# Optimization experiments

Hardware: AMD Instinct MI355X
Metric: run time of the kernel (lower is better)

Reference implementation:

```python
import jax, jax.numpy as jnp
import numpy as np

B, S, D, H, WIN = 2, 2048, 1024, 16, 512
DK = D // H
NEG_INF = float('-inf')


def setup_inputs() -> dict:
    key = jax.random.key(0)
    ks = jax.random.split(key, 9)
    sc = 1.0 / np.sqrt(D)
    def w(k):
        return jax.random.normal(k, (D, D), jnp.float32) * sc
    def b(k):
        return jax.random.normal(k, (D,), jnp.float32) * 0.01
    return {
        'x': jax.random.normal(ks[0], (B, S, D), jnp.float32),
        'Wq_w': w(ks[1]), 'Wq_b': b(jax.random.fold_in(ks[1], 1)),
        'Wk_w': w(ks[2]), 'Wk_b': b(jax.random.fold_in(ks[2], 1)),
        'Wv_w': w(ks[3]), 'Wv_b': b(jax.random.fold_in(ks[3], 1)),
        'Wo_w': w(ks[4]), 'Wo_b': b(jax.random.fold_in(ks[4], 1)),
    }


def _sliding_window_softmax(scores):
    """Faithful port of _apply_sliding_window_attention.

    scores: [B, H, S, S]. seq_len is a multiple of WIN (padding_len == 0,
    which is the only case where the original torch code runs without a
    shape error). Reshape rows/cols into WIN-sized blocks, apply the full
    causal mask (viewed block-wise), softmax over the within-window key
    axis, reshape back. Rows whose entire window block is masked produce
    NaN in torch; here they are defined as 0 (safe softmax) so the
    reference is numerically usable.
    """
    b, h, s, _ = scores.shape
    nb = s // WIN
    causal = jnp.tril(jnp.ones((s, s), dtype=bool)).reshape(1, 1, nb, WIN, nb, WIN)
    sc = scores.reshape(b, h, nb, WIN, nb, WIN)
    sc = jnp.where(causal, sc, NEG_INF)
    m = jnp.max(sc, axis=-1, keepdims=True)
    e = jnp.exp(sc - jnp.where(jnp.isfinite(m), m, 0.0))
    e = jnp.where(causal, e, 0.0)
    denom = jnp.sum(e, axis=-1, keepdims=True)
    probs = e / jnp.where(denom == 0.0, 1.0, denom)
    return probs.reshape(b, h, s, s)


def reference(x, Wq_w, Wq_b, Wk_w, Wk_b, Wv_w, Wv_b, Wo_w, Wo_b):
    b, s, d = x.shape
    # torch nn.Linear: y = x @ W.T + b
    q = (x @ Wq_w.T + Wq_b).reshape(b, s, H, DK).transpose(0, 2, 1, 3)  # [B,H,S,DK]
    k = (x @ Wk_w.T + Wk_b).reshape(b, s, H, DK).transpose(0, 2, 1, 3)
    v = (x @ Wv_w.T + Wv_b).reshape(b, s, H, DK).transpose(0, 2, 1, 3)

    attn_scores = jnp.einsum('bhqd,bhkd->bhqk', q, k) / np.sqrt(DK)  # [B,H,S,S]
    if WIN < s:  # sliding-window branch (window softmax, as in the source)
        attn_scores = _sliding_window_softmax(attn_scores)
    # second, full-row softmax (the source applies softmax again)
    attn_probs = jax.nn.softmax(attn_scores, axis=-1)
    attn_out = jnp.einsum('bhqk,bhkd->bhqd', attn_probs, v)
    attn_out = attn_out.transpose(0, 2, 1, 3).reshape(b, s, d)
    return attn_out @ Wo_w.T + Wo_b
```

## Files before the change

kernel.cpp:

```cpp
#include <hip/hip_runtime.h>
#include <hip/hip_bf16.h>

typedef short v8s __attribute__((ext_vector_type(8)));
typedef float v4f __attribute__((ext_vector_type(4)));
typedef unsigned int v4u __attribute__((ext_vector_type(4)));
typedef unsigned int v2u __attribute__((ext_vector_type(2)));

#define DEV static __device__ __forceinline__
#define AS1 __attribute__((address_space(1)))
#define AS3 __attribute__((address_space(3)))

DEV float bf2f(unsigned short u){ unsigned int x=((unsigned int)u)<<16; float f; __builtin_memcpy(&f,&x,4); return f; }
DEV short f2bf(float f){ __hip_bfloat16 h=__float2bfloat16(f); short s; __builtin_memcpy(&s,&h,2); return s; }
DEV unsigned int f2bfu(float f){ unsigned int u; __builtin_memcpy(&u,&f,4); return (u + 0x7fffu + ((u>>16)&1u)) >> 16; }
DEV unsigned int pk2(float a, float b){ return f2bfu(a) | (f2bfu(b)<<16); }
DEV v4f mfma16(v8s a, v8s b, v4f c){ return __builtin_amdgcn_mfma_f32_16x16x32_bf16(a,b,c,0,0,0); }
DEV float fexp2(float x){
#if __has_builtin(__builtin_amdgcn_exp2f)
  return __builtin_amdgcn_exp2f(x);
#else
  float r; asm("v_exp_f32 %0, %1" : "=v"(r) : "v"(x)); return r;
#endif
}

__global__ __launch_bounds__(256) void convert_kernel(
    const float* __restrict__ x,  const float* __restrict__ Wq,
    const float* __restrict__ Wk, const float* __restrict__ Wv,
    short* __restrict__ xb, short* __restrict__ wqb,
    short* __restrict__ wkb, short* __restrict__ wvb)
{
  unsigned g = blockIdx.x*256u + threadIdx.x;
  const float* src; short* dst; unsigned off;
  if (g < 1048576u){ src=x;  dst=xb;  off=g; }
  else if (g < 1310720u){ src=Wq; dst=wqb; off=g-1048576u; }
  else if (g < 1572864u){ src=Wk; dst=wkb; off=g-1310720u; }
  else { src=Wv; dst=wvb; off=g-1572864u; }
  v4f f = *(const v4f*)(src + (size_t)off*4);
  v2u r; r[0]=pk2(f[0],f[1]); r[1]=pk2(f[2],f[3]);
  *(v2u*)(dst + (size_t)off*4) = r;
}

__global__ __launch_bounds__(256) void convertW_kernel(const float* __restrict__ src,
                                                       short* __restrict__ dst)
{
  unsigned off = blockIdx.x*256u + threadIdx.x;
  v4f f = *(const v4f*)(src + (size_t)off*4);
  v2u r; r[0]=pk2(f[0],f[1]); r[1]=pk2(f[2],f[3]);
  *(v2u*)(dst + (size_t)off*4) = r;
}

DEV void gemm_core16(const short* __restrict__ A, const short* __restrict__ Bmat,
                     int brow0, int bn0, int tid, short* As, short* Bs, v4f acc[4][4])
{
  const int l = tid & 63, w = tid >> 6;
  const int wr = (w>>1)*64, wc = (w&1)*64;
  const int row = tid>>2, p = tid&3;
  const int sw = (p^((row>>1)&3))*8;
  auto STAGE=[&](int kt,int buf){
    const short* a0 = A    + (size_t)(brow0+row   )*1024 + kt*32 + sw;
    const short* a1 = A    + (size_t)(brow0+row+64)*1024 + kt*32 + sw;
    const short* b0 = Bmat + (size_t)(bn0 +row   )*1024 + kt*32 + sw;
    const short* b1 = Bmat + (size_t)(bn0 +row+64)*1024 + kt*32 + sw;
    __builtin_amdgcn_global_load_lds((const AS1 void*)a0,(AS3 void*)(As+buf*4096+(size_t)tid*8),16,0,0);
    __builtin_amdgcn_global_load_lds((const AS1 void*)a1,(AS3 void*)(As+buf*4096+(size_t)(tid+256)*8),16,0,0);
    __builtin_amdgcn_global_load_lds((const AS1 void*)b0,(AS3 void*)(Bs+buf*4096+(size_t)tid*8),16,0,0);
    __builtin_amdgcn_global_load_lds((const AS1 void*)b1,(AS3 void*)(Bs+buf*4096+(size_t)(tid+256)*8),16,0,0);
  };
  STAGE(0,0);
  asm volatile("s_waitcnt vmcnt(0)" ::: "memory");
  __builtin_amdgcn_s_barrier();
  int cur=0;
  for (int kt=0; kt<32; ++kt){
    if (kt<31) STAGE(kt+1,cur^1);
    v8s af[4], bfr[4];
    #pragma unroll
    for (int m=0;m<4;++m){ int r=wr+m*16+(l&15); af[m]=*(const v8s*)&As[cur*4096+(r*4+((l>>4)^((r>>1)&3)))*8]; }
    #pragma unroll
    for (int n=0;n<4;++n){ int r=wc+n*16+(l&15); bfr[n]=*(const v8s*)&Bs[cur*4096+(r*4+((l>>4)^((r>>1)&3)))*8]; }
    #pragma unroll
    for (int m=0;m<4;++m)
      #pragma unroll
      for (int n=0;n<4;++n)
        acc[m][n]=mfma16(af[m],bfr[n],acc[m][n]);
    asm volatile("s_waitcnt vmcnt(0)" ::: "memory");
    __builtin_amdgcn_s_barrier();
    cur^=1;
  }
}

__global__ __launch_bounds__(256) void qkv_gemm(const short* __restrict__ xb,
    const short* __restrict__ wqb, const short* __restrict__ wkb, const short* __restrict__ wvb,
    const float* __restrict__ bq, const float* __restrict__ bk, const float* __restrict__ bv,
    short* __restrict__ qo, short* __restrict__ ko, short* __restrict__ vfo)
{
  __shared__ short As[8192], Bs[8192];
  const int tid=threadIdx.x, l=tid&63, w=tid>>6;
  const int bcol0=blockIdx.x*128, brow0=blockIdx.y*128;
  const int mat=bcol0>>10, n0=bcol0&1023;
  const short* Wm   = mat==0?wqb:(mat==1?wkb:wvb);
  const float* bias = mat==0?bq:(mat==1?bk:bv);
  v4f acc[4][4];
  v4f vz={0.f,0.f,0.f,0.f};
  #pragma unroll
  for(int m=0;m<4;++m)
    #pragma unroll
    for(int n=0;n<4;++n) acc[m][n]=vz;
  gemm_core16(xb, Wm, brow0, n0, tid, As, Bs, acc);
  const int wr=(w>>1)*64, wc=(w&1)*64;
  const float qscale = 0.18033688011112042f;
  #pragma unroll
  for(int m=0;m<4;++m)
  #pragma unroll
  for(int n=0;n<4;++n)
  #pragma unroll
  for(int r=0;r<4;++r){
    int row=brow0+wr+m*16+(l>>4)*4+r;
    int col=n0+wc+n*16+(l&15);
    float v=acc[m][n][r]+bias[col];
    int b=row>>11, s=row&2047, h=col>>6, dk=col&63;
    int bh=b*16+h;
    if(mat==0)      qo[((size_t)bh*2048+s)*64+dk]=f2bf(v*qscale);
    else if(mat==1) ko[((size_t)bh*2048+s)*64+dk]=f2bf(v);
    else{
      int kb=s>>9, c=(s>>5)&15, ki=s&31;
      int g2=(ki>>2)&3, j=(ki>>4)*4+(ki&3);
      int lane2=g2*16+(dk&15);
      vfo[((((size_t)bh*4+kb)*16+c)*4+(size_t)(dk>>4))*512 + lane2*8 + j]=f2bf(v);
    }
  }
}

__global__ __launch_bounds__(256) void vbsum_kernel(const short* __restrict__ vf, float* __restrict__ vbp)
{
  __shared__ float red[4][4][16];
  const int bh=blockIdx.x, kb=blockIdx.y, tid=threadIdx.x, wv=tid>>6, l=tid&63;
  const short* base = vf + ((size_t)(bh*4+kb))*16*4*512;
  float acc[4]={0.f,0.f,0.f,0.f};
  #pragma unroll
  for(int cc=0;cc<4;++cc){
    int c=wv*4+cc;
    #pragma unroll
    for(int dt=0;dt<4;++dt){
      v8s vv=*(const v8s*)(base + ((size_t)(c*4+dt))*512 + l*8);
      float s=0.f;
      #pragma unroll
      for(int j=0;j<8;++j) s+=bf2f((unsigned short)vv[j]);
      acc[dt]+=s;
    }
  }
  #pragma unroll
  for(int dt=0;dt<4;++dt){
    acc[dt]+=__shfl_xor(acc[dt],16);
    acc[dt]+=__shfl_xor(acc[dt],32);
  }
  if(l<16){
    #pragma unroll
    for(int dt=0;dt<4;++dt) red[wv][dt][l]=acc[dt];
  }
  __syncthreads();
  if(tid<64){
    int dt=tid>>4, d=tid&15;
    float s=(red[0][dt][d]+red[1][dt][d])+(red[2][dt][d]+red[3][dt][d]);
    vbp[(size_t)(bh*4+kb)*64 + dt*16 + d]=s;
  }
}

__global__ __launch_bounds__(256) void attn_kernel(
  const short* __restrict__ q, const short* __restrict__ k, const short* __restrict__ vf,
  const float* __restrict__ vbp, short* __restrict__ attn)
{
  __shared__ short kbuf[16384];
  __shared__ float d1buf[256];
  const int tid=threadIdx.x, l=tid&63, wv=tid>>6;
  const int bh=blockIdx.x, qt=31-blockIdx.y;
  const int qb=qt>>3;
  const int qrow0=qt*64+wv*16;
  const int g=l>>4, q16=l&15;
  const int b=bh>>4, h=bh&15;
  const int qglob=qrow0+q16;
  const int lrow=wv*16+q16;

  const short* qbase = q + (size_t)bh*2048*64;
  const short* kbase = k + (size_t)bh*2048*64;
  const short* qp = qbase + (size_t)(qrow0+q16)*64 + g*8;
  v8s qa0=*(const v8s*)qp, qa1=*(const v8s*)(qp+32);
  v4f vz={0.f,0.f,0.f,0.f};

  auto stage=[&](int kb2,int hb2){
    #pragma unroll
    for (int i=0;i<8;++i){
      int idx=i*256+tid, key=idx>>3, p=idx&7, pp=p^(key&7);
      const short* gp = kbase + (size_t)(kb2*512+hb2*256+key)*64 + pp*8;
      __builtin_amdgcn_global_load_lds((const AS1 void*)gp,
          (AS3 void*)((char*)kbuf + idx*16), 16, 0, 0);
    }
  };

#define QKE(CT, EV)                                                     \
  v4f EV;                                                               \
  { int krow=((CT)&15)*16+q16;                                          \
    int s0=g^(krow&7), s1=(g+4)^(krow&7);                               \
    v8s k0=*(const v8s*)&kbuf[(krow*8+s0)*8];                           \
    v8s k1=*(const v8s*)&kbuf[(krow*8+s1)*8];                           \
    __builtin_amdgcn_s_setprio(1);                                      \
    v4f t=mfma16(k0,qa0,vz);                                            \
    v4f e4=mfma16(k1,qa1,t);                                            \
    __builtin_amdgcn_s_setprio(0);                                      \
    _Pragma("unroll")                                                   \
    for (int r=0;r<4;++r){                                              \
      float s=e4[r];                                                    \
      if (diag && kb*512+(CT)*16+g*4+r > qglob) s=-1e38f;               \
      EV[r]=fexp2(s);                                                   \
    }                                                                   \
  }

  for (int kb=0; kb<=qb; ++kb){
    const bool diag=(kb==qb);
    const int tmaxw = diag ? ((qt&7)*4+wv) : 31;
    const int blkhi = diag ? ((qt&7)*4+3) : 31;
    float d1acc=0.f;
    stage(kb,0); __syncthreads();
    #pragma unroll
    for (int ct=0;ct<16;++ct) if (ct<=tmaxw){
      QKE(ct,ev)
      d1acc+=(ev[0]+ev[1])+(ev[2]+ev[3]);
    }
    __syncthreads();
    if (blkhi>=16){
      stage(kb,1); __syncthreads();
      #pragma unroll
      for (int ct=16;ct<32;++ct) if (ct<=tmaxw){
        QKE(ct,ev)
        d1acc+=(ev[0]+ev[1])+(ev[2]+ev[3]);
      }
      __syncthreads();
    }
    float d1=d1acc;
    d1+=__shfl_xor(d1,16); d1+=__shfl_xor(d1,32);
    if (l<16) d1buf[(wv*16+l)*4+kb]=1.44269504f/d1;
  }
  __syncthreads();

  v4f o[4];
  #pragma unroll
  for(int dt=0;dt<4;++dt) o[dt]=vz;
  float zacc=0.f;

#define CHUNK(C)                                                        \
  { QKE(2*(C),eA) QKE(2*(C)+1,eB)                                       \
    float w0=fexp2(eA[0]*d1i)-1.0f, w1=fexp2(eA[1]*d1i)-1.0f;           \
    float w2=fexp2(eA[2]*d1i)-1.0f, w3=fexp2(eA[3]*d1i)-1.0f;           \
    float w4=fexp2(eB[0]*d1i)-1.0f, w5=fexp2(eB[1]*d1i)-1.0f;           \
    float w6=fexp2(eB[2]*d1i)-1.0f, w7=fexp2(eB[3]*d1i)-1.0f;           \
    zacc+=((w0+w1)+(w2+w3))+((w4+w5)+(w6+w7));                          \
    union { v4u u; v8s s; } pa;                                         \
    pa.u[0]=pk2(w0,w1); pa.u[1]=pk2(w2,w3);                             \
    pa.u[2]=pk2(w4,w5); pa.u[3]=pk2(w6,w7);                             \
    const short* vfp = vf + ((((size_t)bh*4+kb)*16+(C))*4)*512 + l*8;   \
    __builtin_amdgcn_s_setprio(1);                                      \
    _Pragma("unroll")                                                   \
    for (int dt=0;dt<4;++dt){                                           \
      v8s vfr=*(const v8s*)(vfp + (size_t)dt*512);                      \
      o[dt]=mfma16(pa.s,vfr,o[dt]);                                     \
    }                                                                   \
    __builtin_amdgcn_s_setprio(0);                                      \
  }

  for (int kb=0; kb<=qb; ++kb){
    const bool diag=(kb==qb);
    const int tmaxw = diag ? ((qt&7)*4+wv) : 31;
    const int blkhi = diag ? ((qt&7)*4+3) : 31;
    const float d1i=d1buf[lrow*4+kb];
    stage(kb,0); __syncthreads();
    #pragma unroll
    for (int c=0;c<8;++c) if (2*c<=tmaxw) CHUNK(c)
    __syncthreads();
    if (blkhi>=16){
      stage(kb,1); __syncthreads();
      #pragma unroll
      for (int c=8;c<16;++c) if (2*c<=tmaxw) CHUNK(c)
      __syncthreads();
    }
  }
#undef CHUNK
#undef QKE

  float z=zacc;
  z+=__shfl_xor(z,16); z+=__shfl_xor(z,32);
  float base[4];
  #pragma unroll
  for (int dt=0;dt<4;++dt){
    float s=0.f;
    #pragma unroll
    for (int kk=0;kk<4;++kk) s+=vbp[(size_t)(bh*4+kk)*64 + dt*16 + q16];
    base[dt]=s;
  }
  #pragma unroll
  for (int r=0;r<4;++r){
    float zr=__shfl(z, g*4+r);
    float inv=1.0f/(2048.0f+zr);
    int rowi=qrow0+g*4+r;
    size_t obase=((size_t)b*2048+rowi)*1024 + h*64;
    #pragma unroll
    for (int dt=0;dt<4;++dt)
      attn[obase + dt*16 + q16] = f2bf((o[dt][r]+base[dt])*inv);
  }
}

__global__ __launch_bounds__(256) void oproj_gemm(const short* __restrict__ at,
    const short* __restrict__ wob, const float* __restrict__ bo, float* __restrict__ out)
{
  __shared__ short As[8192], Bs[8192];
  const int tid=threadIdx.x, l=tid&63, w=tid>>6;
  const int bcol0=blockIdx.x*128, brow0=blockIdx.y*128;
  v4f acc[4][4];
  v4f vz={0.f,0.f,0.f,0.f};
  #pragma unroll
  for(int m=0;m<4;++m)
    #pragma unroll
    for(int n=0;n<4;++n) acc[m][n]=vz;
  gemm_core16(at, wob, brow0, bcol0, tid, As, Bs, acc);
  const int wr=(w>>1)*64, wc=(w&1)*64;
  #pragma unroll
  for(int m=0;m<4;++m)
  #pragma unroll
  for(int n=0;n<4;++n)
  #pragma unroll
  for(int r=0;r<4;++r){
    int row=brow0+wr+m*16+(l>>4)*4+r;
    int col=bcol0+wc+n*16+(l&15);
    out[(size_t)row*1024+col]=acc[m][n][r]+bo[col];
  }
}

extern "C" void kernel_launch(void* const* d_in, const int* in_sizes, int n_in,
                              void* d_out, int out_size, void* d_ws, size_t ws_size,
                              hipStream_t stream)
{
  const float* x  =(const float*)d_in[0];
  const float* Wq =(const float*)d_in[1];
  const float* bq =(const float*)d_in[2];
  const float* Wk =(const float*)d_in[3];
  const float* bk =(const float*)d_in[4];
  const float* Wv =(const float*)d_in[5];
  const float* bv =(const float*)d_in[6];
  const float* Wo =(const float*)d_in[7];
  const float* bo =(const float*)d_in[8];
  float* out=(float*)d_out;
  char* ws=(char*)d_ws;
  short* xb_ws =(short*)(ws);
  short* at_ws =(short*)(ws);
  short* q_ws  =(short*)(ws + ((size_t)8<<20));
  short* wob_ws=(short*)(ws + ((size_t)8<<20));
  short* k_ws  =(short*)(ws + ((size_t)16<<20));
  short* vf_ws =(short*)(ws + ((size_t)24<<20));
  char*  outb  =(char*)d_out;
  short* wqb   =(short*)(outb);
  short* wkb   =(short*)(outb + ((size_t)2<<20));
  short* wvb   =(short*)(outb + ((size_t)4<<20));
  float* vbp_ws=(float*)(outb + ((size_t)7<<20));

  convert_kernel<<<dim3(7168),256,0,stream>>>(x,Wq,Wk,Wv,xb_ws,wqb,wkb,wvb);
  qkv_gemm<<<dim3(24,32),256,0,stream>>>(xb_ws,wqb,wkb,wvb,bq,bk,bv,q_ws,k_ws,vf_ws);
  vbsum_kernel<<<dim3(32,4),256,0,stream>>>(vf_ws,vbp_ws);
  attn_kernel<<<dim3(32,32),256,0,stream>>>(q_ws,k_ws,vf_ws,vbp_ws,at_ws);
  convertW_kernel<<<dim3(1024),256,0,stream>>>(Wo,wob_ws);
  oproj_gemm<<<dim3(8,32),256,0,stream>>>(at_ws,wob_ws,bo,out);
}
```

Baseline: 152.1 us.

## Cache window scores in registers as bf16 instead of recomputing QK in second pass

The attention kernel previously ran two passes over each key window: one computing QK^T and exp to get the row denominators, and a second recomputing QK^T to build the PV weights. Now the single pass keeps the exponentiated scores packed as bf16 in a 64-entry register array, reduces the denominator, then runs PV directly from the cached values. This removes half the K staging, barriers and QK MFMAs, and also drops the s_setprio hints. In exchange it adds heavy register pressure (64 extra VGPRs, possibly spilling to scratch or lowering occupancy) and rounds the intermediate scores to bf16 before the second exponent.

```diff
diff --git a/kernel.cpp b/kernel.cpp
--- a/kernel.cpp
+++ b/kernel.cpp
@@ -170,7 +170,6 @@
   const float* __restrict__ vbp, short* __restrict__ attn)
 {
   __shared__ short kbuf[16384];
-  __shared__ float d1buf[256];
   const int tid=threadIdx.x, l=tid&63, wv=tid>>6;
   const int bh=blockIdx.x, qt=31-blockIdx.y;
   const int qb=qt>>3;
@@ -178,7 +177,6 @@
   const int g=l>>4, q16=l&15;
   const int b=bh>>4, h=bh&15;
   const int qglob=qrow0+q16;
-  const int lrow=wv*16+q16;
 
   const short* qbase = q + (size_t)bh*2048*64;
   const short* kbase = k + (size_t)bh*2048*64;
@@ -196,94 +194,76 @@
     }
   };
 
-#define QKE(CT, EV)                                                     \
-  v4f EV;                                                               \
+  v4f o[4];
+  #pragma unroll
+  for(int dt=0;dt<4;++dt) o[dt]=vz;
+  float zacc=0.f;
+  unsigned sc16[64];
+
+#define QKE(CT)                                                         \
   { int krow=((CT)&15)*16+q16;                                          \
     int s0=g^(krow&7), s1=(g+4)^(krow&7);                               \
     v8s k0=*(const v8s*)&kbuf[(krow*8+s0)*8];                           \
     v8s k1=*(const v8s*)&kbuf[(krow*8+s1)*8];                           \
-    __builtin_amdgcn_s_setprio(1);                                      \
     v4f t=mfma16(k0,qa0,vz);                                            \
     v4f e4=mfma16(k1,qa1,t);                                            \
-    __builtin_amdgcn_s_setprio(0);                                      \
+    v4f ev;                                                             \
     _Pragma("unroll")                                                   \
     for (int r=0;r<4;++r){                                              \
       float s=e4[r];                                                    \
       if (diag && kb*512+(CT)*16+g*4+r > qglob) s=-1e38f;               \
-      EV[r]=fexp2(s);                                                   \
+      ev[r]=fexp2(s);                                                   \
+      d1acc+=ev[r];                                                     \
     }                                                                   \
-  }
-
-  for (int kb=0; kb<=qb; ++kb){
-    const bool diag=(kb==qb);
-    const int tmaxw = diag ? ((qt&7)*4+wv) : 31;
-    const int blkhi = diag ? ((qt&7)*4+3) : 31;
-    float d1acc=0.f;
-    stage(kb,0); __syncthreads();
-    #pragma unroll
-    for (int ct=0;ct<16;++ct) if (ct<=tmaxw){
-      QKE(ct,ev)
-      d1acc+=(ev[0]+ev[1])+(ev[2]+ev[3]);
-    }
-    __syncthreads();
-    if (blkhi>=16){
-      stage(kb,1); __syncthreads();
-      #pragma unroll
-      for (int ct=16;ct<32;++ct) if (ct<=tmaxw){
-        QKE(ct,ev)
-        d1acc+=(ev[0]+ev[1])+(ev[2]+ev[3]);
-      }
-      __syncthreads();
-    }
-    float d1=d1acc;
-    d1+=__shfl_xor(d1,16); d1+=__shfl_xor(d1,32);
-    if (l<16) d1buf[(wv*16+l)*4+kb]=1.44269504f/d1;
-  }
-  __syncthreads();
-
-  v4f o[4];
-  #pragma unroll
-  for(int dt=0;dt<4;++dt) o[dt]=vz;
-  float zacc=0.f;
-
-#define CHUNK(C)                                                        \
-  { QKE(2*(C),eA) QKE(2*(C)+1,eB)                                       \
-    float w0=fexp2(eA[0]*d1i)-1.0f, w1=fexp2(eA[1]*d1i)-1.0f;           \
-    float w2=fexp2(eA[2]*d1i)-1.0f, w3=fexp2(eA[3]*d1i)-1.0f;           \
-    float w4=fexp2(eB[0]*d1i)-1.0f, w5=fexp2(eB[1]*d1i)-1.0f;           \
-    float w6=fexp2(eB[2]*d1i)-1.0f, w7=fexp2(eB[3]*d1i)-1.0f;           \
+    sc16[(CT)*2]=pk2(ev[0],ev[1]); sc16[(CT)*2+1]=pk2(ev[2],ev[3]);     \
+  }
+
+#define PVC(C)                                                          \
+  { unsigned a0=sc16[4*(C)], a1=sc16[4*(C)+1];                          \
+    unsigned b0=sc16[4*(C)+2], b1=sc16[4*(C)+3];                        \
+    float w0=fexp2(bf2f((unsigned short)(a0&0xffffu))*d1i)-1.0f;        \
+    float w1=fexp2(bf2f((unsigned short)(a0>>16))   *d1i)-1.0f;        \
+    float w2=fexp2(bf2f((unsigned short)(a1&0xffffu))*d1i)-1.0f;        \
+    float w3=fexp2(bf2f((unsigned short)(a1>>16))   *d1i)-1.0f;        \
+    float w4=fexp2(bf2f((unsigned short)(b0&0xffffu))*d1i)-1.0f;        \
+    float w5=fexp2(bf2f((unsigned short)(b0>>16))   *d1i)-1.0f;        \
+    float w6=fexp2(bf2f((unsigned short)(b1&0xffffu))*d1i)-1.0f;        \
+    float w7=fexp2(bf2f((unsigned short)(b1>>16))   *d1i)-1.0f;        \
     zacc+=((w0+w1)+(w2+w3))+((w4+w5)+(w6+w7));                          \
     union { v4u u; v8s s; } pa;                                         \
     pa.u[0]=pk2(w0,w1); pa.u[1]=pk2(w2,w3);                             \
     pa.u[2]=pk2(w4,w5); pa.u[3]=pk2(w6,w7);                             \
     const short* vfp = vf + ((((size_t)bh*4+kb)*16+(C))*4)*512 + l*8;   \
-    __builtin_amdgcn_s_setprio(1);                                      \
     _Pragma("unroll")                                                   \
     for (int dt=0;dt<4;++dt){                                           \
       v8s vfr=*(const v8s*)(vfp + (size_t)dt*512);                      \
       o[dt]=mfma16(pa.s,vfr,o[dt]);                                     \
     }                                                                   \
-    __builtin_amdgcn_s_setprio(0);                                      \
   }
 
   for (int kb=0; kb<=qb; ++kb){
     const bool diag=(kb==qb);
-    const int tmaxw = diag ? ((qt&7)*4+wv) : 31;
+    const int tmax2 = diag ? (((qt&7)*4+wv)|1) : 31;
     const int blkhi = diag ? ((qt&7)*4+3) : 31;
-    const float d1i=d1buf[lrow*4+kb];
+    float d1acc=0.f;
     stage(kb,0); __syncthreads();
     #pragma unroll
-    for (int c=0;c<8;++c) if (2*c<=tmaxw) CHUNK(c)
+    for (int ct=0;ct<16;++ct) if (ct<=tmax2) QKE(ct)
     __syncthreads();
     if (blkhi>=16){
       stage(kb,1); __syncthreads();
       #pragma unroll
-      for (int c=8;c<16;++c) if (2*c<=tmaxw) CHUNK(c)
+      for (int ct=16;ct<32;++ct) if (ct<=tmax2) QKE(ct)
       __syncthreads();
     }
-  }
-#undef CHUNK
+    float d1=d1acc;
+    d1+=__shfl_xor(d1,16); d1+=__shfl_xor(d1,32);
+    const float d1i=1.44269504f/d1;
+    #pragma unroll
+    for (int c=0;c<16;++c) if (2*c<=tmax2) PVC(c)
+  }
 #undef QKE
+#undef PVC
 
   float z=zacc;
   z+=__shfl_xor(z,16); z+=__shfl_xor(z,32);
```

New measurement: 151.6 us, median of 2. No clear change (-0.3%).
